# Kernel optimization log

Measured on AMD Instinct MI355X. Metric: run time of the kernel, lower is better.

The kernel has to match this reference:

```python
import math
import jax, jax.numpy as jnp
import numpy as np

N = 256          # num_spins
DIM = 64         # vector dimension of each spin
BETA = 1.0
MAX_ITER = 40    # solver_fwd_max_iter
TOL = 1e-4       # solver_fwd_tol
J_STD = 1.0 / np.sqrt(N * DIM * 2)


def _J_eff(J_raw):
    # symmetrize + traceless, as in VectorSpinModel.J()
    J = 0.5 * (J_raw + J_raw.T)
    return J * (1.0 - jnp.eye(N, dtype=J.dtype))


def _V_and_inv(t, J):
    # t: (b, 1) -> expand to (b, N); V = diag_embed(t) - J
    b = t.shape[0]
    tfull = jnp.broadcast_to(t, (b, N))
    V = jnp.eye(N, dtype=t.dtype) * tfull[:, :, None] - J[None]  # (b, N, N)
    I = jnp.broadcast_to(jnp.eye(N, dtype=t.dtype), V.shape)
    V_inv = jnp.linalg.solve(V, I)
    return tfull, V, V_inv


def _grad_t_phi(t, h, J, beta):
    # scalar-t branch: t has shape (b, 1)
    _, _, V_inv = _V_and_inv(t, J)
    tr = jnp.trace(V_inv, axis1=-2, axis2=-1)                     # (b,)
    y = V_inv @ h                                                  # (b, N, f)
    z = V_inv @ y                                                  # V_inv @ V_inv @ h
    quad = jnp.sum(h * z, axis=(-2, -1))                           # h^T Vinv Vinv h
    g = beta * N - 0.5 * tr - beta / (4.0 * DIM) * quad            # (b,)
    return g[:, None]


def _newton(t0, h, J, beta):
    def g(t):
        return _grad_t_phi(t, h, J, beta)

    def step(t, _):
        f, df = jax.jvp(g, (t,), (jnp.ones_like(t),))
        upd = jnp.where(jnp.abs(f) > TOL, f / df, jnp.zeros_like(f))
        return t - upd, None

    t_star, _ = jax.lax.scan(step, t0, None, length=MAX_ITER)
    return t_star


def _phi(t, h, J, beta):
    tfull, V, V_inv = _V_and_inv(t, J)
    _, logabsdet = jnp.linalg.slogdet(V)
    quad = jnp.sum(h * (V_inv @ h), axis=(-2, -1))  # einsum bif,bij,bjf->b
    return beta * tfull.sum(-1) - 0.5 * logabsdet + beta / (4.0 * DIM) * quad


def setup_inputs() -> dict:
    key = jax.random.key(0)
    k1, k2 = jax.random.split(key)
    x = jax.random.normal(k1, (64, N, DIM), dtype=jnp.float32)
    J_raw = jax.random.normal(k2, (N, N), dtype=jnp.float32) * J_STD
    return {"x": x, "J_raw": J_raw}


def reference(x, J_raw):
    J = _J_eff(J_raw)
    h = x  # _prepare_sources is identity
    t0 = jnp.ones((x.shape[0], 1), dtype=x.dtype)
    t_star = _newton(t0, h, J, BETA)
    phi = _phi(t_star, h, J, BETA)
    afe = -(1.0 / BETA) * (0.5 * jnp.log(jnp.asarray(math.pi / BETA, x.dtype)) + phi / N)
    return afe, jax.lax.stop_gradient(t_star)
```

## Files before the change

### kernel.cpp

```cpp
#include <hip/hip_runtime.h>
#include <math.h>

#define NN 256
#define DIMF 64
#define BATCH 64
#define PB 4
#define NB (BATCH + PB)
#define KMAX 12
#define NM (KMAX + 1)
#define NSTEPS (KMAX / 2)
#define CG 4
#define CW 16
#define YSTR 264

using short4v = __attribute__((ext_vector_type(4))) short;
using short8  = __attribute__((ext_vector_type(8))) short;
using f32x4   = __attribute__((ext_vector_type(4))) float;

__device__ __forceinline__ float bf2f(unsigned short u) {
    union { unsigned int i; float f; } v; v.i = ((unsigned int)u) << 16; return v.f;
}
__device__ __forceinline__ unsigned short f2bf(float f) {
    union { float f; unsigned int i; } v; v.f = f;
    unsigned int b = v.i;
    return (unsigned short)((b + 0x7FFFu + ((b >> 16) & 1u)) >> 16);
}

__global__ void jbuild_kernel(const float* __restrict__ Jr,
                              unsigned short* __restrict__ Jb,
                              float* __restrict__ m) {
    int i = blockIdx.x * 256 + threadIdx.x;
    int r = i >> 8, c = i & 255;
    float v = (r == c) ? 0.0f : 0.5f * (Jr[i] + Jr[(c << 8) + r]);
    Jb[((c >> 3) << 11) + (r << 3) + (c & 7)] = f2bf(v);
    if (i < NB * NM) m[i] = 0.0f;
}

__global__ __launch_bounds__(512, 4)
void chain_kernel(const unsigned short* __restrict__ J,
                  const float* __restrict__ x,
                  float* __restrict__ m) {
    __shared__ __align__(16) unsigned short ybuf[2][CW][YSTR];
    const int g = blockIdx.x;
    const int b = blockIdx.y;
    const int t = threadIdx.x;
    const int w = t >> 6;
    const int lane = t & 63;
    const int quad = lane >> 4;
    const int l15 = lane & 15;

    short8 jreg[2][8];
    #pragma unroll
    for (int mt = 0; mt < 2; ++mt) {
        const int row = w * 32 + mt * 16 + l15;
        #pragma unroll
        for (int kc = 0; kc < 8; ++kc)
            jreg[mt][kc] = *(const short8*)(J + ((((kc << 2) | quad) << 11) + (row << 3)));
    }

    if (b < BATCH) {
        const float* xb = x + (b << 14) + (g << 4);
        float s0 = 0.f;
        #pragma unroll
        for (int it = 0; it < 2; ++it) {
            const int idx = it * 512 + t;
            const int k = idx >> 2;
            const int nn = (idx & 3) << 2;
            const float4 v = *(const float4*)(xb + (k << 6) + nn);
            s0 += v.x * v.x + v.y * v.y + v.z * v.z + v.w * v.w;
            ybuf[0][nn + 0][k] = f2bf(v.x);
            ybuf[0][nn + 1][k] = f2bf(v.y);
            ybuf[0][nn + 2][k] = f2bf(v.z);
            ybuf[0][nn + 3][k] = f2bf(v.w);
        }
        #pragma unroll
        for (int o = 32; o > 0; o >>= 1) s0 += __shfl_down(s0, o);
        if (lane == 0) atomicAdd(&m[b * NM], s0);
    } else {
        const int p = b - BATCH;
        #pragma unroll
        for (int i = t; i < CW * 256; i += 512) {
            const int c = i >> 8, k = i & 255;
            ybuf[0][c][k] = (k == p * 64 + g * 16 + c) ? 0x3F80 : 0;
        }
    }
    __syncthreads();

    int cur = 0;
    for (int j = 1; j <= NSTEPS; ++j) {
        f32x4 acc0 = {}, acc1 = {};
        #pragma unroll
        for (int kc = 0; kc < 8; ++kc) {
            const int kb = kc * 32 + quad * 8;
            const short8 bfrag = *(const short8*)&ybuf[cur][l15][kb];
            acc0 = __builtin_amdgcn_mfma_f32_16x16x32_bf16(jreg[0][kc], bfrag, acc0, 0, 0, 0);
            acc1 = __builtin_amdgcn_mfma_f32_16x16x32_bf16(jreg[1][kc], bfrag, acc1, 0, 0, 0);
        }

        const int nxt = cur ^ 1;
        float d1 = 0.f, d2 = 0.f;
        #pragma unroll
        for (int mt = 0; mt < 2; ++mt) {
            const int rb = w * 32 + mt * 16 + quad * 4;
            const short4v yp = *(const short4v*)&ybuf[cur][l15][rb];
            short4v yn;
            #pragma unroll
            for (int r = 0; r < 4; ++r) {
                const float v = (mt == 0) ? acc0[r] : acc1[r];
                d1 += bf2f((unsigned short)yp[r]) * v;
                d2 += v * v;
                yn[r] = (short)f2bf(v);
            }
            if (j < NSTEPS) *(short4v*)&ybuf[nxt][l15][rb] = yn;
        }
        #pragma unroll
        for (int o = 32; o > 0; o >>= 1) {
            d1 += __shfl_down(d1, o);
            d2 += __shfl_down(d2, o);
        }
        if (lane == 0) {
            atomicAdd(&m[b * NM + 2 * j - 1], d1);
            atomicAdd(&m[b * NM + 2 * j],     d2);
        }
        cur = nxt;
        __syncthreads();
    }
}

__global__ void solve_kernel(const float* __restrict__ m, float* __restrict__ out) {
    int b = threadIdx.x;
    if (b >= BATCH) return;
    float mk[NM], Tk[NM];
    mk[0] = m[b * NM];
    Tk[0] = 256.0f;
    for (int k = 1; k < NM; ++k) {
        mk[k] = m[b * NM + k];
        float s = 0.f;
        for (int p = 0; p < PB; ++p) s += m[(BATCH + p) * NM + k];
        Tk[k] = s;
    }
    float t = 1.0f;
    for (int it = 0; it < 40; ++it) {
        float inv = 1.0f / t;
        float p1 = inv, S1 = 0.f, S1d = 0.f, S3 = 0.f, S3d = 0.f;
        for (int k = 0; k < NM; ++k) {
            float p2 = p1 * inv;
            float p3 = p2 * inv;
            float kp1 = (float)(k + 1);
            S1  += Tk[k] * p1;
            S1d += kp1 * Tk[k] * p2;
            S3  += kp1 * mk[k] * p2;
            S3d += kp1 * (float)(k + 2) * mk[k] * p3;
            p1 = p2;
        }
        float f  = 256.0f - 0.5f * S1 - S3 * (1.0f / 256.0f);
        float df = 0.5f * S1d + S3d * (1.0f / 256.0f);
        if (fabsf(f) <= 1e-4f) break;
        t -= f / df;
    }
    float inv = 1.0f / t;
    float logdet = 256.0f * logf(t);
    float quad = 0.f;
    float p1 = inv, pk = 1.0f;
    for (int k = 0; k < NM; ++k) {
        quad += mk[k] * p1;
        if (k >= 1) { pk *= inv; logdet -= Tk[k] / (float)k * pk; }
        p1 *= inv;
    }
    float phi = 256.0f * t - 0.5f * logdet + quad * (1.0f / 256.0f);
    float afe = -(0.5f * logf((float)M_PI) + phi * (1.0f / 256.0f));
    out[b] = afe;
    out[BATCH + b] = t;
}

extern "C" void kernel_launch(void* const* d_in, const int* in_sizes, int n_in,
                              void* d_out, int out_size, void* d_ws, size_t ws_size,
                              hipStream_t stream) {
    const float* x  = (const float*)d_in[0];
    const float* Jr = (const float*)d_in[1];
    float* out = (float*)d_out;

    char* base = (char*)d_ws;
    unsigned short* Jb = (unsigned short*)base;
    float* m = (float*)(base + 131072);

    jbuild_kernel<<<256, 256, 0, stream>>>(Jr, Jb, m);
    chain_kernel<<<dim3(CG, NB), 512, 0, stream>>>(Jb, x, m);
    solve_kernel<<<1, 64, 0, stream>>>(m, out);
}
```

Before: 74.21 us.

## Fold probe-vector chains into batch blocks and fuse solve via last-block counter

The trace-estimation probe chains, previously separate blocks, now ride along in the first PB batch blocks as a second 16-column tile sharing the same J fragments, so the grid shrinks from 68 to 64 rows. The separate solve kernel launch is removed: each block increments an atomic counter and the last block to finish runs the Newton solve. This cuts one kernel launch and the straggler blocks, but the first blocks do double MFMA work and occupancy is lowered through the launch bounds and larger shared buffer.

```diff
diff --git a/kernel.cpp b/kernel.cpp
--- a/kernel.cpp
+++ b/kernel.cpp
@@ -12,6 +12,8 @@
 #define CG 4
 #define CW 16
 #define YSTR 264
+#define NBLOCKS (CG * BATCH)
+#define CTR_IDX (NB * NM)
 
 using short4v = __attribute__((ext_vector_type(4))) short;
 using short8  = __attribute__((ext_vector_type(8))) short;
@@ -33,17 +35,15 @@
     int r = i >> 8, c = i & 255;
     float v = (r == c) ? 0.0f : 0.5f * (Jr[i] + Jr[(c << 8) + r]);
     Jb[((c >> 3) << 11) + (r << 3) + (c & 7)] = f2bf(v);
-    if (i < NB * NM) m[i] = 0.0f;
-}
-
-__global__ __launch_bounds__(512, 4)
-void chain_kernel(const unsigned short* __restrict__ J,
-                  const float* __restrict__ x,
-                  float* __restrict__ m) {
-    __shared__ __align__(16) unsigned short ybuf[2][CW][YSTR];
-    const int g = blockIdx.x;
-    const int b = blockIdx.y;
-    const int t = threadIdx.x;
+    if (i <= CTR_IDX) m[i] = 0.0f;
+}
+
+template<int NT>
+__device__ __forceinline__ void chain_body(const unsigned short* __restrict__ J,
+                                           const float* __restrict__ x,
+                                           float* __restrict__ m,
+                                           unsigned short (*ybuf)[2 * CW][YSTR],
+                                           int g, int b, int t) {
     const int w = t >> 6;
     const int lane = t & 63;
     const int quad = lane >> 4;
@@ -58,7 +58,7 @@
             jreg[mt][kc] = *(const short8*)(J + ((((kc << 2) | quad) << 11) + (row << 3)));
     }
 
-    if (b < BATCH) {
+    {
         const float* xb = x + (b << 14) + (g << 4);
         float s0 = 0.f;
         #pragma unroll
@@ -76,67 +76,87 @@
         #pragma unroll
         for (int o = 32; o > 0; o >>= 1) s0 += __shfl_down(s0, o);
         if (lane == 0) atomicAdd(&m[b * NM], s0);
-    } else {
-        const int p = b - BATCH;
-        #pragma unroll
+    }
+    if (NT == 2) {
+        const int base = b * 64 + g * 16;
         for (int i = t; i < CW * 256; i += 512) {
             const int c = i >> 8, k = i & 255;
-            ybuf[0][c][k] = (k == p * 64 + g * 16 + c) ? 0x3F80 : 0;
+            ybuf[0][CW + c][k] = (k == base + c) ? 0x3F80 : 0;
         }
     }
     __syncthreads();
 
     int cur = 0;
     for (int j = 1; j <= NSTEPS; ++j) {
-        f32x4 acc0 = {}, acc1 = {};
+        f32x4 acc[NT][2];
+        #pragma unroll
+        for (int nt = 0; nt < NT; ++nt) { acc[nt][0] = (f32x4){}; acc[nt][1] = (f32x4){}; }
         #pragma unroll
         for (int kc = 0; kc < 8; ++kc) {
             const int kb = kc * 32 + quad * 8;
-            const short8 bfrag = *(const short8*)&ybuf[cur][l15][kb];
-            acc0 = __builtin_amdgcn_mfma_f32_16x16x32_bf16(jreg[0][kc], bfrag, acc0, 0, 0, 0);
-            acc1 = __builtin_amdgcn_mfma_f32_16x16x32_bf16(jreg[1][kc], bfrag, acc1, 0, 0, 0);
+            #pragma unroll
+            for (int nt = 0; nt < NT; ++nt) {
+                const short8 bfrag = *(const short8*)&ybuf[cur][nt * CW + l15][kb];
+                acc[nt][0] = __builtin_amdgcn_mfma_f32_16x16x32_bf16(jreg[0][kc], bfrag, acc[nt][0], 0, 0, 0);
+                acc[nt][1] = __builtin_amdgcn_mfma_f32_16x16x32_bf16(jreg[1][kc], bfrag, acc[nt][1], 0, 0, 0);
+            }
         }
 
         const int nxt = cur ^ 1;
-        float d1 = 0.f, d2 = 0.f;
-        #pragma unroll
-        for (int mt = 0; mt < 2; ++mt) {
-            const int rb = w * 32 + mt * 16 + quad * 4;
-            const short4v yp = *(const short4v*)&ybuf[cur][l15][rb];
-            short4v yn;
+        float d1[NT], d2[NT];
+        #pragma unroll
+        for (int nt = 0; nt < NT; ++nt) {
+            d1[nt] = 0.f; d2[nt] = 0.f;
             #pragma unroll
-            for (int r = 0; r < 4; ++r) {
-                const float v = (mt == 0) ? acc0[r] : acc1[r];
-                d1 += bf2f((unsigned short)yp[r]) * v;
-                d2 += v * v;
-                yn[r] = (short)f2bf(v);
-            }
-            if (j < NSTEPS) *(short4v*)&ybuf[nxt][l15][rb] = yn;
+            for (int mt = 0; mt < 2; ++mt) {
+                const int rb = w * 32 + mt * 16 + quad * 4;
+                const short4v yp = *(const short4v*)&ybuf[cur][nt * CW + l15][rb];
+                short4v yn;
+                #pragma unroll
+                for (int r = 0; r < 4; ++r) {
+                    const float v = acc[nt][mt][r];
+                    d1[nt] += bf2f((unsigned short)yp[r]) * v;
+                    d2[nt] += v * v;
+                    yn[r] = (short)f2bf(v);
+                }
+                if (j < NSTEPS) *(short4v*)&ybuf[nxt][nt * CW + l15][rb] = yn;
+            }
         }
         #pragma unroll
         for (int o = 32; o > 0; o >>= 1) {
-            d1 += __shfl_down(d1, o);
-            d2 += __shfl_down(d2, o);
+            #pragma unroll
+            for (int nt = 0; nt < NT; ++nt) {
+                d1[nt] += __shfl_down(d1[nt], o);
+                d2[nt] += __shfl_down(d2[nt], o);
+            }
         }
         if (lane == 0) {
-            atomicAdd(&m[b * NM + 2 * j - 1], d1);
-            atomicAdd(&m[b * NM + 2 * j],     d2);
+            atomicAdd(&m[b * NM + 2 * j - 1], d1[0]);
+            atomicAdd(&m[b * NM + 2 * j],     d2[0]);
+            if (NT == 2) {
+                atomicAdd(&m[(BATCH + b) * NM + 2 * j - 1], d1[1]);
+                atomicAdd(&m[(BATCH + b) * NM + 2 * j],     d2[1]);
+            }
         }
         cur = nxt;
         __syncthreads();
     }
 }
 
-__global__ void solve_kernel(const float* __restrict__ m, float* __restrict__ out) {
-    int b = threadIdx.x;
+__device__ __forceinline__ float mload(const float* p) {
+    return __hip_atomic_load(p, __ATOMIC_RELAXED, __HIP_MEMORY_SCOPE_AGENT);
+}
+
+__device__ void solve_body(const float* __restrict__ m, float* __restrict__ out) {
+    const int b = threadIdx.x;
     if (b >= BATCH) return;
     float mk[NM], Tk[NM];
-    mk[0] = m[b * NM];
+    mk[0] = mload(&m[b * NM]);
     Tk[0] = 256.0f;
     for (int k = 1; k < NM; ++k) {
-        mk[k] = m[b * NM + k];
+        mk[k] = mload(&m[b * NM + k]);
         float s = 0.f;
-        for (int p = 0; p < PB; ++p) s += m[(BATCH + p) * NM + k];
+        for (int p = 0; p < PB; ++p) s += mload(&m[(BATCH + p) * NM + k]);
         Tk[k] = s;
     }
     float t = 1.0f;
@@ -173,6 +193,32 @@
     out[BATCH + b] = t;
 }
 
+__global__ __launch_bounds__(512, 2)
+void chain_kernel(const unsigned short* __restrict__ J,
+                  const float* __restrict__ x,
+                  float* __restrict__ m,
+                  float* __restrict__ out) {
+    __shared__ __align__(16) unsigned short ybuf[2][2 * CW][YSTR];
+    __shared__ int lastFlag;
+    const int g = blockIdx.x;
+    const int b = blockIdx.y;
+    const int t = threadIdx.x;
+
+    if (b < PB) chain_body<2>(J, x, m, ybuf, g, b, t);
+    else        chain_body<1>(J, x, m, ybuf, g, b, t);
+
+    if (t == 0) {
+        __threadfence();
+        int prev = atomicAdd((int*)&m[CTR_IDX], 1);
+        lastFlag = (prev == NBLOCKS - 1);
+    }
+    __syncthreads();
+    if (lastFlag) {
+        __threadfence();
+        solve_body(m, out);
+    }
+}
+
 extern "C" void kernel_launch(void* const* d_in, const int* in_sizes, int n_in,
                               void* d_out, int out_size, void* d_ws, size_t ws_size,
                               hipStream_t stream) {
@@ -185,6 +231,5 @@
     float* m = (float*)(base + 131072);
 
     jbuild_kernel<<<256, 256, 0, stream>>>(Jr, Jb, m);
-    chain_kernel<<<dim3(CG, NB), 512, 0, stream>>>(Jb, x, m);
-    solve_kernel<<<1, 64, 0, stream>>>(m, out);
-}
+    chain_kernel<<<dim3(CG, BATCH), 512, 0, stream>>>(Jb, x, m, out);
+}
```

After: 77.15 us. 1.04x slower.
